# Kernel optimization log

Hardware: AMD Instinct MI355X
Metric: run time of the kernel (lower is better)

The kernel has to match this reference:

```python
import jax, jax.numpy as jnp
import numpy as np

MAX_INT = 1e4  # sentinel used by the original (transitions into START / out of STOP forbidden)
VOCAB, E, H, T, B, S = 50257, 512, 1024, 50, 8, 512  # T = tagset_size + 2


def _lstm_scan(x, h0, c0, Wih, Whh, b):
    # x: [time, batch, E] (time axis is the ORIGINAL batch dim, faithful to the
    # torch code which feeds [B,S,E] into a batch_first=False LSTM)
    def step(carry, xt):
        h, c = carry
        g = xt @ Wih.T + h @ Whh.T + b
        i, f, gg, o = jnp.split(g, 4, axis=-1)  # torch gate order i,f,g,o
        c = jax.nn.sigmoid(f) * c + jax.nn.sigmoid(i) * jnp.tanh(gg)
        h = jax.nn.sigmoid(o) * jnp.tanh(c)
        return (h, c), h
    _, hs = jax.lax.scan(step, (h0, c0), x)
    return hs


def setup_inputs() -> dict:
    key = jax.random.key(0)
    k = jax.random.split(key, 14)
    Hd = H // 2
    X = jax.random.randint(k[0], (B, S), 0, VOCAB)
    Y = jax.random.randint(k[1], (B, S), 0, T - 2)  # real tags only (no start/stop)
    h0 = jax.random.normal(k[2], (2, S, Hd), jnp.float32)
    c0 = jax.random.normal(k[3], (2, S, Hd), jnp.float32)
    emb_table = jax.random.normal(k[4], (VOCAB, E), jnp.float32) * 0.02
    Wih_f = jax.random.normal(k[5], (4 * Hd, E), jnp.float32) * 0.05
    Whh_f = jax.random.normal(k[6], (4 * Hd, Hd), jnp.float32) * 0.05
    b_f = jnp.zeros((4 * Hd,), jnp.float32)
    Wih_b = jax.random.normal(k[7], (4 * Hd, E), jnp.float32) * 0.05
    Whh_b = jax.random.normal(k[8], (4 * Hd, Hd), jnp.float32) * 0.05
    b_b = jnp.zeros((4 * Hd,), jnp.float32)
    fc_W = jax.random.normal(k[9], (T, H), jnp.float32) * 0.05
    fc_b = jnp.zeros((T,), jnp.float32)
    tr = jax.random.normal(k[10], (T, T), jnp.float32)
    transitions = tr.at[-2, :].set(-MAX_INT).at[:, -1].set(-MAX_INT)
    return {"X": X, "Y": Y, "h0": h0, "c0": c0, "emb_table": emb_table,
            "Wih_f": Wih_f, "Whh_f": Whh_f, "b_f": b_f,
            "Wih_b": Wih_b, "Whh_b": Whh_b, "b_b": b_b,
            "fc_W": fc_W, "fc_b": fc_b, "transitions": transitions}


def reference(X, Y, h0, c0, emb_table, Wih_f, Whh_f, b_f, Wih_b, Whh_b, b_b, fc_W, fc_b, transitions):
    emb = emb_table[X]                                   # [B,S,E]
    # BiLSTM: torch sees axis0 as time (faithful quirk), hidden batch == S
    hf = _lstm_scan(emb, h0[0], c0[0], Wih_f, Whh_f, b_f)
    hb = _lstm_scan(emb[::-1], h0[1], c0[1], Wih_b, Whh_b, b_b)[::-1]
    lstm_out = jnp.concatenate([hf, hb], axis=-1)        # [B,S,H]
    feats = lstm_out @ fc_W.T + fc_b                     # [B,S,T]
    nB, Tt = X.shape[0], transitions.shape[0]
    # CRF forward algorithm (log partition), vectorized over tags
    init = jnp.full((nB, Tt), -MAX_INT, feats.dtype).at[:, -2].set(0.0)
    def crf_step(fv, feat):                              # fv [B,T], feat [B,T]
        nv = fv[:, None, :] + transitions[None, :, :] + feat[:, :, None]  # [B,next,prev]
        return jax.nn.logsumexp(nv, axis=2), None
    fv, _ = jax.lax.scan(crf_step, init, jnp.swapaxes(feats, 0, 1))
    forward_score = jax.nn.logsumexp(fv + transitions[-1][None, :], axis=1).sum()
    # gold path score
    start = jnp.full((nB, 1), Tt - 2, dtype=Y.dtype)
    tags = jnp.concatenate([start, Y], axis=1)           # [B,S+1]
    trans_sc = transitions[tags[:, 1:], tags[:, :-1]].sum()
    emit_sc = jnp.take_along_axis(feats, tags[:, 1:, None], axis=2)[..., 0].sum()
    gold_score = trans_sc + emit_sc + transitions[-1, tags[:, -1]].sum()
    score = forward_score - gold_score
    return score, Y
```

## Files before the change

kernel.cpp:

```cpp
#include <hip/hip_runtime.h>
#include <hip/hip_bf16.h>

typedef __attribute__((ext_vector_type(4))) float f32x4;
typedef __attribute__((ext_vector_type(8))) short short8;

#define LN2F 0.69314718055994531f

__device__ __forceinline__ unsigned short f2b(float x){
  union{float f;unsigned u;}v; v.f=x;
  unsigned r = v.u + 0x7fffu + ((v.u>>16)&1u);
  return (unsigned short)(r>>16);
}
__device__ __forceinline__ float b2f(unsigned short h){
  union{unsigned u;float f;}v; v.u = ((unsigned)h)<<16; return v.f;
}
__device__ __forceinline__ float sigm(float x){ return 1.f/(1.f+__expf(-x)); }
__device__ __forceinline__ float tanh_(float x){ float t=__expf(2.f*x); return 1.f - 2.f/(t+1.f); }

__device__ __forceinline__ void gll16(const void* g, void* l){
  __builtin_amdgcn_global_load_lds((const __attribute__((address_space(1))) void*)g,
                                   (__attribute__((address_space(3))) void*)l, 16, 0, 0);
}

__global__ __launch_bounds__(256) void prep_kernel(
  const int* __restrict__ X, const int* __restrict__ Y,
  const float* __restrict__ h0, const float* __restrict__ c0,
  const float* __restrict__ emb,
  const float* __restrict__ WihF, const float* __restrict__ WihB,
  const float* __restrict__ WhhFf, const float* __restrict__ WhhBf,
  const float* __restrict__ fcWf, const float* __restrict__ trans,
  unsigned short* __restrict__ Abf, unsigned short* __restrict__ Wcat,
  unsigned short* __restrict__ WhhF, unsigned short* __restrict__ WhhB,
  unsigned short* __restrict__ hbufs, float* __restrict__ cbuf,
  unsigned short* __restrict__ fcW, unsigned short* __restrict__ Ebf,
  float* __restrict__ out)
{
  const int tid = blockIdx.x*256 + threadIdx.x;
  const int nth = gridDim.x*256;
  if(tid==0) out[0] = 0.f;
  for(int i=tid;i<524288;i+=nth){
    int r = i>>7, q = i&127;
    float4 v = ((const float4*)(emb + (size_t)X[r]*512))[q];
    ushort4 o; o.x=f2b(v.x); o.y=f2b(v.y); o.z=f2b(v.z); o.w=f2b(v.w);
    ((ushort4*)Abf)[i] = o;
  }
  for(int i=tid;i<524288;i+=nth){
    int r = i>>7, q = i&127;
    const float* src = (r<2048) ? (WihF + (size_t)r*512) : (WihB + (size_t)(r-2048)*512);
    float4 v = ((const float4*)src)[q];
    ushort4 o; o.x=f2b(v.x); o.y=f2b(v.y); o.z=f2b(v.z); o.w=f2b(v.w);
    ((ushort4*)Wcat)[i] = o;
  }
  for(int i=tid;i<262144;i+=nth){
    float4 v = ((const float4*)WhhFf)[i];
    ushort4 o; o.x=f2b(v.x); o.y=f2b(v.y); o.z=f2b(v.z); o.w=f2b(v.w);
    ((ushort4*)WhhF)[i] = o;
  }
  for(int i=tid;i<262144;i+=nth){
    float4 v = ((const float4*)WhhBf)[i];
    ushort4 o; o.x=f2b(v.x); o.y=f2b(v.y); o.z=f2b(v.z); o.w=f2b(v.w);
    ((ushort4*)WhhB)[i] = o;
  }
  for(int i=tid;i<131072;i+=nth){
    int d = i>>16, rest = i&65535;
    float4 v = ((const float4*)h0)[i];
    ushort4 o; o.x=f2b(v.x); o.y=f2b(v.y); o.z=f2b(v.z); o.w=f2b(v.w);
    ((ushort4*)hbufs)[(size_t)(d*2)*65536 + rest] = o;
  }
  for(int i=tid;i<131072;i+=nth) ((float4*)cbuf)[i] = ((const float4*)c0)[i];
  for(int i=tid;i<16384;i+=nth){
    int n = i>>8, q = i&255;
    float4 v;
    if (n<50) v = ((const float4*)(fcWf + (size_t)n*1024))[q];
    else { v.x=0.f; v.y=0.f; v.z=0.f; v.w=0.f; }
    ushort4 o; o.x=f2b(v.x); o.y=f2b(v.y); o.z=f2b(v.z); o.w=f2b(v.w);
    ((ushort4*)fcW)[i] = o;
  }
  for(int i=tid;i<4096;i+=nth){
    int n = i>>6, p = i&63;
    float v = (n<50 && p<50) ? __expf(trans[n*50+p]) : 0.f;
    Ebf[i] = f2b(v);
  }
  for(int i=tid;i<4096;i+=nth) out[1+i] = (float)Y[i];
}

__global__ __launch_bounds__(256) void gemm1_kernel(const unsigned short* __restrict__ A,
                                                    const unsigned short* __restrict__ B,
                                                    unsigned short* __restrict__ C){
  __shared__ __align__(16) unsigned short As[2][128*32];
  __shared__ __align__(16) unsigned short Bs[2][128*32];
  const int t = threadIdx.x, w = t>>6, l = t&63;
  const int m0 = blockIdx.x<<7, n0 = blockIdx.y<<7;
  const int wr = (w>>1)<<6, wc = (w&1)<<6;
  const int fr = l&15, fk = (l>>4)<<3;
  f32x4 acc[4][4];
  #pragma unroll
  for(int i=0;i<4;i++)
    #pragma unroll
    for(int j=0;j<4;j++) acc[i][j]=(f32x4)0.f;
  const unsigned short* Ab = A + (size_t)m0*512;
  const unsigned short* Bb = B + (size_t)n0*512;
  const int r0 = (w<<5) + (l>>2);
  const int c0 = (l&3)<<3;
  const int wo = (w<<5)*32;
  gll16(Ab + (size_t)r0*512 + c0,      As[0] + wo);
  gll16(Ab + (size_t)(r0+16)*512 + c0, As[0] + wo + 16*32);
  gll16(Bb + (size_t)r0*512 + c0,      Bs[0] + wo);
  gll16(Bb + (size_t)(r0+16)*512 + c0, Bs[0] + wo + 16*32);
  asm volatile("s_waitcnt vmcnt(0)" ::: "memory");
  __syncthreads();
  int cur = 0;
  for(int kt=0; kt<16; ++kt){
    if(kt<15){
      const int kc = ((kt+1)<<5) + c0;
      gll16(Ab + (size_t)r0*512 + kc,      As[cur^1] + wo);
      gll16(Ab + (size_t)(r0+16)*512 + kc, As[cur^1] + wo + 16*32);
      gll16(Bb + (size_t)r0*512 + kc,      Bs[cur^1] + wo);
      gll16(Bb + (size_t)(r0+16)*512 + kc, Bs[cur^1] + wo + 16*32);
    }
    short8 af[4], bf[4];
    #pragma unroll
    for(int mi=0;mi<4;mi++) af[mi] = *(const short8*)&As[cur][(wr+mi*16+fr)*32 + fk];
    #pragma unroll
    for(int ni=0;ni<4;ni++) bf[ni] = *(const short8*)&Bs[cur][(wc+ni*16+fr)*32 + fk];
    #pragma unroll
    for(int mi=0;mi<4;mi++)
      #pragma unroll
      for(int ni=0;ni<4;ni++)
        acc[mi][ni] = __builtin_amdgcn_mfma_f32_16x16x32_bf16(af[mi], bf[ni], acc[mi][ni], 0,0,0);
    asm volatile("s_waitcnt vmcnt(0)" ::: "memory");
    __syncthreads();
    cur ^= 1;
  }
  #pragma unroll
  for(int mi=0;mi<4;mi++)
    #pragma unroll
    for(int ni=0;ni<4;ni++)
      #pragma unroll
      for(int j=0;j<4;j++){
        int row = m0 + wr + mi*16 + ((l>>4)<<2) + j;
        int col = n0 + wc + ni*16 + fr;
        C[(size_t)row*4096 + col] = f2b(acc[mi][ni][j]);
      }
}

__global__ __launch_bounds__(256) void lstm_step_kernel(
  unsigned short* __restrict__ hbufs, float* __restrict__ cbuf,
  unsigned short* __restrict__ hall, const unsigned short* __restrict__ Gin,
  const unsigned short* __restrict__ WhhF_, const unsigned short* __restrict__ WhhB_,
  const float* __restrict__ bF, const float* __restrict__ bB, int t)
{
  __shared__ __align__(16) unsigned short WL[16*4*64*8];
  __shared__ __align__(16) unsigned short Ab4[4][128*32];
  const int d = blockIdx.z;
  const int m0 = blockIdx.x<<7;
  const int u0 = blockIdx.y<<4;
  const int tin = d ? (7-t) : t;
  const int par = t&1;
  const unsigned short* hprev = hbufs + (size_t)(d*2+par)*262144;
  unsigned short* hnext = hbufs + (size_t)(d*2+(par^1))*262144;
  const unsigned short* W = d ? WhhB_ : WhhF_;
  const float* bias = d ? bB : bF;
  const int tx = threadIdx.x, w = tx>>6, l = tx&63;
  const int fr = l&15, q = l>>4, fk = q<<3;
  {
    const int row = tx >> 2, qq = tx & 3;
    const int g = row >> 4, ul = row & 15;
    const int grow = (g<<9) + u0 + ul;
    #pragma unroll
    for(int kt=0;kt<16;kt++){
      uint4 v = *(const uint4*)(W + (size_t)grow*512 + kt*32 + qq*8);
      *(uint4*)(WL + ((kt*4+g)*64 + (qq*16+ul))*8) = v;
    }
  }
  __syncthreads();
  f32x4 acc[2][4];
  #pragma unroll
  for(int i=0;i<2;i++)
    #pragma unroll
    for(int j=0;j<4;j++) acc[i][j]=(f32x4)0.f;
  const int r0 = (w<<5) + (l>>2), c0 = (l&3)<<3;
  const unsigned short* hA0 = hprev + (size_t)(m0+r0)*512;
  const unsigned short* hA1 = hprev + (size_t)(m0+r0+16)*512;
#define ABUF(i) (Ab4[(i)] + ((w<<5)*32))
  gll16(hA0 + 0*32 + c0, ABUF(0)); gll16(hA1 + 0*32 + c0, ABUF(0)+16*32);
  gll16(hA0 + 1*32 + c0, ABUF(1)); gll16(hA1 + 1*32 + c0, ABUF(1)+16*32);
  gll16(hA0 + 2*32 + c0, ABUF(2)); gll16(hA1 + 2*32 + c0, ABUF(2)+16*32);
  gll16(hA0 + 3*32 + c0, ABUF(3)); gll16(hA1 + 3*32 + c0, ABUF(3)+16*32);
#define LSTEP(KT, VM) {                                                       \
    if((KT)+4 < 16){                                                          \
      const int kc_ = ((KT)+4)*32 + c0;                                       \
      gll16(hA0 + kc_, ABUF(((KT)+4)&3));                                     \
      gll16(hA1 + kc_, ABUF(((KT)+4)&3)+16*32);                               \
    }                                                                         \
    asm volatile("s_waitcnt vmcnt(" VM ")" ::: "memory");                     \
    const unsigned short* cur_ = ABUF((KT)&3);                                \
    short8 a0_ = *(const short8*)(cur_ + fr*32 + fk);                         \
    short8 a1_ = *(const short8*)(cur_ + (16+fr)*32 + fk);                    \
    short8 bv_[4];                                                            \
    _Pragma("unroll")                                                         \
    for(int g=0;g<4;g++) bv_[g] = *(const short8*)(WL + (((KT)*4+g)*64 + l)*8);\
    _Pragma("unroll")                                                         \
    for(int g=0;g<4;g++){                                                     \
      acc[0][g] = __builtin_amdgcn_mfma_f32_16x16x32_bf16(a0_, bv_[g], acc[0][g], 0,0,0); \
      acc[1][g] = __builtin_amdgcn_mfma_f32_16x16x32_bf16(a1_, bv_[g], acc[1][g], 0,0,0); \
    }                                                                         \
  }
  LSTEP(0,"8")  LSTEP(1,"8")  LSTEP(2,"8")  LSTEP(3,"8")
  LSTEP(4,"8")  LSTEP(5,"8")  LSTEP(6,"8")  LSTEP(7,"8")
  LSTEP(8,"8")  LSTEP(9,"8")  LSTEP(10,"8") LSTEP(11,"8")
  LSTEP(12,"6") LSTEP(13,"4") LSTEP(14,"2") LSTEP(15,"0")
#undef LSTEP
#undef ABUF
  #pragma unroll
  for(int mi=0;mi<2;mi++)
    #pragma unroll
    for(int j=0;j<4;j++){
      int rs = m0 + w*32 + mi*16 + (q<<2) + j;
      int u  = u0 + fr;
      size_t grow = (size_t)(tin*512 + rs)*4096 + (size_t)d*2048;
      float p0 = acc[mi][0][j] + b2f(Gin[grow +    0 + u]) + bias[   0+u];
      float p1 = acc[mi][1][j] + b2f(Gin[grow +  512 + u]) + bias[ 512+u];
      float p2 = acc[mi][2][j] + b2f(Gin[grow + 1024 + u]) + bias[1024+u];
      float p3 = acc[mi][3][j] + b2f(Gin[grow + 1536 + u]) + bias[1536+u];
      size_t ci = (size_t)d*262144 + (size_t)rs*512 + u;
      float c = sigm(p1)*cbuf[ci] + sigm(p0)*tanh_(p2);
      cbuf[ci] = c;
      float h = sigm(p3)*tanh_(c);
      hnext[(size_t)rs*512+u] = f2b(h);
      hall[(size_t)(tin*512+rs)*1024 + (size_t)d*512 + u] = f2b(h);
    }
}

__global__ __launch_bounds__(256) void fc_kernel(const unsigned short* __restrict__ hA,
    const unsigned short* __restrict__ Wf, const float* __restrict__ fcb,
    float* __restrict__ feats){
  __shared__ __align__(16) unsigned short As[128*40];
  __shared__ __align__(16) unsigned short Bs[64*40];
  const int tx = threadIdx.x, w = tx>>6, l = tx&63;
  const int m0 = blockIdx.x<<7;
  const int srow = tx>>2, scol = (tx&3)<<3;
  const int fr=l&15, fk=(l>>4)<<3;
  f32x4 acc[2][4];
  #pragma unroll
  for(int i=0;i<2;i++)
    #pragma unroll
    for(int j=0;j<4;j++) acc[i][j]=(f32x4)0.f;
  uint4 pa0 = *(const uint4*)(hA + (size_t)(m0+srow)*1024 + scol);
  uint4 pa1 = *(const uint4*)(hA + (size_t)(m0+64+srow)*1024 + scol);
  uint4 pb0 = *(const uint4*)(Wf + (size_t)srow*1024 + scol);
  for(int kt=0; kt<32; ++kt){
    __syncthreads();
    *(uint4*)&As[srow*40+scol] = pa0;
    *(uint4*)&As[(64+srow)*40+scol] = pa1;
    *(uint4*)&Bs[srow*40+scol] = pb0;
    __syncthreads();
    if(kt<31){
      int kc = (kt+1)*32 + scol;
      pa0 = *(const uint4*)(hA + (size_t)(m0+srow)*1024 + kc);
      pa1 = *(const uint4*)(hA + (size_t)(m0+64+srow)*1024 + kc);
      pb0 = *(const uint4*)(Wf + (size_t)srow*1024 + kc);
    }
    short8 af[2], bf[4];
    #pragma unroll
    for(int mi=0;mi<2;mi++) af[mi] = *(const short8*)&As[(w*32+mi*16+fr)*40 + fk];
    #pragma unroll
    for(int ni=0;ni<4;ni++) bf[ni] = *(const short8*)&Bs[(ni*16+fr)*40 + fk];
    #pragma unroll
    for(int mi=0;mi<2;mi++)
      #pragma unroll
      for(int ni=0;ni<4;ni++)
        acc[mi][ni] = __builtin_amdgcn_mfma_f32_16x16x32_bf16(af[mi], bf[ni], acc[mi][ni], 0,0,0);
  }
  #pragma unroll
  for(int mi=0;mi<2;mi++)
    #pragma unroll
    for(int ni=0;ni<4;ni++)
      #pragma unroll
      for(int j=0;j<4;j++){
        int rs = m0 + w*32 + mi*16 + ((l>>4)<<2) + j;
        int n  = ni*16 + fr;
        feats[(size_t)rs*64+n] = acc[mi][ni][j] + (n<50 ? fcb[n] : 0.f);
      }
}

__global__ __launch_bounds__(64) void crf_group_kernel(
    const float* __restrict__ feats, const unsigned short* __restrict__ Ebf,
    float* __restrict__ Wout, int* __restrict__ kexp)
{
  __shared__ __align__(16) unsigned short PT[64*72];
  __shared__ float fe[16*64];
  const int g = blockIdx.x, b = blockIdx.y;
  const int l = threadIdx.x;
  const int lj = l & 15, q = l >> 4;
  const float* fb = feats + (size_t)(b*512 + g*16)*64;
  #pragma unroll
  for(int j=0;j<16;j++) fe[j*64 + l] = fb[j*64 + l];
  short8 afE[4][2];
  #pragma unroll
  for(int i=0;i<4;i++)
    #pragma unroll
    for(int h=0;h<2;h++)
      afE[i][h] = *(const short8*)(Ebf + (i*16+lj)*64 + h*32 + q*8);
  {
    uint4 erow[8];
    #pragma unroll
    for(int i=0;i<8;i++) erow[i] = *(const uint4*)(Ebf + l*64 + i*8);
    float ef0 = __expf(fe[l]);
    const unsigned* e32 = (const unsigned*)erow;
    #pragma unroll
    for(int m=0;m<64;m++){
      unsigned short eb = (unsigned short)(e32[m>>1] >> ((m&1)*16));
      PT[m*72 + l] = f2b(b2f(eb) * ef0);
    }
  }
  float sc_lag = 1.f;
  int exprev = 0, kblk = 0;
  #pragma unroll
  for(int k=1;k<16;k++){
    kblk += exprev;
    float ev[4][4];
    #pragma unroll
    for(int i=0;i<4;i++)
      #pragma unroll
      for(int r=0;r<4;r++)
        ev[i][r] = __expf(fe[k*64 + i*16 + q*4 + r]) * sc_lag;
    short8 bfP[4][2];
    #pragma unroll
    for(int j=0;j<4;j++)
      #pragma unroll
      for(int h=0;h<2;h++)
        bfP[j][h] = *(const short8*)&PT[(j*16+lj)*72 + h*32 + q*8];
    f32x4 acc[4][4];
    #pragma unroll
    for(int i=0;i<4;i++)
      #pragma unroll
      for(int j=0;j<4;j++) acc[i][j] = (f32x4)0.f;
    #pragma unroll
    for(int h=0;h<2;h++)
      #pragma unroll
      for(int i=0;i<4;i++)
        #pragma unroll
        for(int j=0;j<4;j++)
          acc[i][j] = __builtin_amdgcn_mfma_f32_16x16x32_bf16(afE[i][h], bfP[j][h], acc[i][j], 0,0,0);
    float mx = 1e-30f;
    float* Wo = Wout + (size_t)(b*32 + g)*4096;
    #pragma unroll
    for(int i=0;i<4;i++)
      #pragma unroll
      for(int j=0;j<4;j++){
        float v0 = acc[i][j][0]*ev[i][0];
        float v1 = acc[i][j][1]*ev[i][1];
        float v2 = acc[i][j][2]*ev[i][2];
        float v3 = acc[i][j][3]*ev[i][3];
        mx = fmaxf(fmaxf(mx, fmaxf(v0,v1)), fmaxf(v2,v3));
        int base = (j*16+lj)*72 + i*16 + q*4;
        *(unsigned*)&PT[base]   = (unsigned)f2b(v0) | ((unsigned)f2b(v1)<<16);
        *(unsigned*)&PT[base+2] = (unsigned)f2b(v2) | ((unsigned)f2b(v3)<<16);
        if(k==15){
          int n = i*16 + q*4, m = j*16 + lj;
          Wo[(size_t)(n+0)*64 + m] = v0;
          Wo[(size_t)(n+1)*64 + m] = v1;
          Wo[(size_t)(n+2)*64 + m] = v2;
          Wo[(size_t)(n+3)*64 + m] = v3;
        }
      }
    #pragma unroll
    for(int off=1; off<64; off<<=1) mx = fmaxf(mx, __shfl_xor(mx, off));
    int ex = ((__builtin_bit_cast(int, mx) >> 23) & 0xff) - 127;
    ex = ex < -120 ? -120 : (ex > 120 ? 120 : ex);
    sc_lag = __builtin_bit_cast(float, (unsigned)((127-ex)<<23));
    exprev = ex;
  }
  if(l==0) kexp[b*32 + g] = kblk;
}

__global__ __launch_bounds__(256) void crf_seq_kernel(const float* __restrict__ W,
    const int* __restrict__ kexp, const float* __restrict__ trans,
    const float* __restrict__ feats, const int* __restrict__ Y,
    float* __restrict__ out){
  const int b = blockIdx.x;
  if(b < 8){
    if(threadIdx.x >= 64) return;
    __shared__ __align__(16) float sh[64];
    const int l = threadIdx.x;
    const float* Wb = W + (size_t)b*131072;
    float kl = (l<32) ? (float)kexp[b*32 + l] : 0.f;
    #pragma unroll
    for(int off=32;off;off>>=1) kl += __shfl_down(kl, off);
    float G = (l==48) ? 1.f : 0.f;
    float sc = 1.f, Mrun = 0.f;
    int exprev = 0;
    float4 curA[16], curB[16];
    #pragma unroll
    for(int i=0;i<16;i++) curA[i] = ((const float4*)(Wb + (size_t)l*64))[i];

#define SEQ_STEP(CUR, NXT, GI) {                                            \
    sh[l] = G;                                                              \
    const float* wn = Wb + (size_t)(((GI)+1)&31)*4096 + (size_t)l*64;       \
    _Pragma("unroll")                                                       \
    for(int i=0;i<16;i++) NXT[i] = ((const float4*)wn)[i];                  \
    float4 gq[16];                                                          \
    _Pragma("unroll")                                                       \
    for(int i=0;i<16;i++) gq[i] = ((const float4*)sh)[i];                   \
    float a0=0.f,a1=0.f,a2=0.f,a3=0.f;                                      \
    _Pragma("unroll")                                                       \
    for(int i=0;i<16;i++){                                                  \
      a0 = fmaf(CUR[i].x, gq[i].x, a0);                                     \
      a1 = fmaf(CUR[i].y, gq[i].y, a1);                                     \
      a2 = fmaf(CUR[i].z, gq[i].z, a2);                                     \
      a3 = fmaf(CUR[i].w, gq[i].w, a3);                                     \
    }                                                                       \
    float S = (a0+a1)+(a2+a3);                                              \
    Mrun += (float)exprev;                                                  \
    G = S * sc;                                                             \
    float Sp = __builtin_bit_cast(float, __builtin_amdgcn_readfirstlane(    \
                 __builtin_bit_cast(int, fmaxf(S, 1e-35f))));               \
    int ex = ((__builtin_bit_cast(int, Sp) >> 23) & 0xff) - 127;            \
    ex = ex < -120 ? -120 : (ex > 120 ? 120 : ex);                          \
    sc = __builtin_bit_cast(float, (unsigned)((127-ex)<<23));               \
    exprev = ex;                                                            \
  }

    for(int g=0; g<32; g+=2){
      SEQ_STEP(curA, curB, g)
      SEQ_STEP(curB, curA, g+1)
    }
#undef SEQ_STEP
    float u = (l<50) ? __expf(trans[49*50+l]) : 0.f;
    float val = G * u;
    #pragma unroll
    for(int off=32;off;off>>=1) val += __shfl_down(val, off);
    if(l==0) atomicAdd(out, logf(fmaxf(val,1e-35f)) + (Mrun + kl)*LN2F);
  } else {
    const int tx = threadIdx.x;
    float acc = 0.f;
    for(int i=tx; i<4096; i+=256){
      int s = i & 511;
      int y = Y[i];
      int prev = s ? Y[i-1] : 48;
      acc += trans[y*50+prev] + feats[(size_t)i*64+y];
      if (s==511) acc += trans[49*50+y];
    }
    #pragma unroll
    for(int off=32; off; off>>=1) acc += __shfl_down(acc, off);
    __shared__ float red[4];
    if((tx&63)==0) red[tx>>6] = acc;
    __syncthreads();
    if(tx==0) atomicAdd(out, -(red[0]+red[1]+red[2]+red[3]));
  }
}

extern "C" void kernel_launch(void* const* d_in, const int* in_sizes, int n_in,
                              void* d_out, int out_size, void* d_ws, size_t ws_size,
                              hipStream_t stream) {
  (void)in_sizes; (void)n_in; (void)out_size; (void)ws_size;
  const int*   X     = (const int*)d_in[0];
  const int*   Y     = (const int*)d_in[1];
  const float* h0    = (const float*)d_in[2];
  const float* c0    = (const float*)d_in[3];
  const float* emb   = (const float*)d_in[4];
  const float* WihF  = (const float*)d_in[5];
  const float* WhhFf = (const float*)d_in[6];
  const float* bF    = (const float*)d_in[7];
  const float* WihB  = (const float*)d_in[8];
  const float* WhhBf = (const float*)d_in[9];
  const float* bB    = (const float*)d_in[10];
  const float* fcWf  = (const float*)d_in[11];
  const float* fcb   = (const float*)d_in[12];
  const float* trans = (const float*)d_in[13];
  float* out = (float*)d_out;
  char* ws = (char*)d_ws;

  unsigned short* Abf   = (unsigned short*)(ws + 0);
  unsigned short* Wcat  = (unsigned short*)(ws + 4194304);
  unsigned short* WhhF  = (unsigned short*)(ws + 8388608);
  unsigned short* WhhB  = (unsigned short*)(ws + 10485760);
  unsigned short* Gin   = (unsigned short*)(ws + 12582912);
  float*          Wgrp  = (float*)(ws + 12582912);
  int*            kexp  = (int*)(ws + 20971520);
  unsigned short* hbufs = (unsigned short*)(ws + 46137344);
  float*          cbuf  = (float*)(ws + 48234496);
  unsigned short* hall  = (unsigned short*)(ws + 50331648);
  unsigned short* fcW   = (unsigned short*)(ws + 58720256);
  float*          feats = (float*)(ws + 58851328);
  unsigned short* Ebf   = (unsigned short*)(ws + 59900160);

  hipLaunchKernelGGL(prep_kernel, dim3(1024), dim3(256), 0, stream,
      X, Y, h0, c0, emb, WihF, WihB, WhhFf, WhhBf, fcWf, trans,
      Abf, Wcat, WhhF, WhhB, hbufs, cbuf, fcW, Ebf, out);
  hipLaunchKernelGGL(gemm1_kernel, dim3(32,32), dim3(256), 0, stream, Abf, Wcat, Gin);
  for(int t=0;t<8;t++)
    hipLaunchKernelGGL(lstm_step_kernel, dim3(4,32,2), dim3(256), 0, stream,
        hbufs, cbuf, hall, Gin, WhhF, WhhB, bF, bB, t);
  hipLaunchKernelGGL(fc_kernel, dim3(32), dim3(256), 0, stream, hall, fcW, fcb, feats);
  hipLaunchKernelGGL(crf_group_kernel, dim3(32,8), dim3(64), 0, stream, feats, Ebf, Wgrp, kexp);
  hipLaunchKernelGGL(crf_seq_kernel, dim3(9), dim3(256), 0, stream, Wgrp, kexp, trans, feats, Y, out);
}
```

Measured before the change: 189.4 us.

## Deepen gemm1 pipeline with per-wave buffers, adjust LSTM prefetch, regroup CRF chunks

The input-projection GEMM now gives each wave its own 4-deep LDS ring and issues loads three stages ahead. This removes the block-wide __syncthreads and keeps more loads in flight, at the cost of each wave loading its own 64-row A and B panels instead of sharing 128-row tiles. The LSTM step prefetch depth drops from 4 to 3 stages. The CRF group kernel now processes 32-step chunks in 16 groups rather than 16-step chunks in 32 groups, which halves the serial steps in the sequential combine kernel but lengthens each group's serial chain.

```diff
diff --git a/kernel.cpp b/kernel.cpp
--- a/kernel.cpp
+++ b/kernel.cpp
@@ -87,51 +87,55 @@
 __global__ __launch_bounds__(256) void gemm1_kernel(const unsigned short* __restrict__ A,
                                                     const unsigned short* __restrict__ B,
                                                     unsigned short* __restrict__ C){
-  __shared__ __align__(16) unsigned short As[2][128*32];
-  __shared__ __align__(16) unsigned short Bs[2][128*32];
+  __shared__ __align__(16) unsigned short SS[4][4][2][2048];
   const int t = threadIdx.x, w = t>>6, l = t&63;
   const int m0 = blockIdx.x<<7, n0 = blockIdx.y<<7;
   const int wr = (w>>1)<<6, wc = (w&1)<<6;
   const int fr = l&15, fk = (l>>4)<<3;
+  const int sr = l>>2, c0 = (l&3)<<3;
   f32x4 acc[4][4];
   #pragma unroll
   for(int i=0;i<4;i++)
     #pragma unroll
     for(int j=0;j<4;j++) acc[i][j]=(f32x4)0.f;
-  const unsigned short* Ab = A + (size_t)m0*512;
-  const unsigned short* Bb = B + (size_t)n0*512;
-  const int r0 = (w<<5) + (l>>2);
-  const int c0 = (l&3)<<3;
-  const int wo = (w<<5)*32;
-  gll16(Ab + (size_t)r0*512 + c0,      As[0] + wo);
-  gll16(Ab + (size_t)(r0+16)*512 + c0, As[0] + wo + 16*32);
-  gll16(Bb + (size_t)r0*512 + c0,      Bs[0] + wo);
-  gll16(Bb + (size_t)(r0+16)*512 + c0, Bs[0] + wo + 16*32);
-  asm volatile("s_waitcnt vmcnt(0)" ::: "memory");
-  __syncthreads();
-  int cur = 0;
-  for(int kt=0; kt<16; ++kt){
-    if(kt<15){
-      const int kc = ((kt+1)<<5) + c0;
-      gll16(Ab + (size_t)r0*512 + kc,      As[cur^1] + wo);
-      gll16(Ab + (size_t)(r0+16)*512 + kc, As[cur^1] + wo + 16*32);
-      gll16(Bb + (size_t)r0*512 + kc,      Bs[cur^1] + wo);
-      gll16(Bb + (size_t)(r0+16)*512 + kc, Bs[cur^1] + wo + 16*32);
-    }
-    short8 af[4], bf[4];
-    #pragma unroll
-    for(int mi=0;mi<4;mi++) af[mi] = *(const short8*)&As[cur][(wr+mi*16+fr)*32 + fk];
-    #pragma unroll
-    for(int ni=0;ni<4;ni++) bf[ni] = *(const short8*)&Bs[cur][(wc+ni*16+fr)*32 + fk];
-    #pragma unroll
-    for(int mi=0;mi<4;mi++)
-      #pragma unroll
-      for(int ni=0;ni<4;ni++)
-        acc[mi][ni] = __builtin_amdgcn_mfma_f32_16x16x32_bf16(af[mi], bf[ni], acc[mi][ni], 0,0,0);
-    asm volatile("s_waitcnt vmcnt(0)" ::: "memory");
-    __syncthreads();
-    cur ^= 1;
-  }
+  const unsigned short* Aw = A + (size_t)(m0+wr)*512;
+  const unsigned short* Bw = B + (size_t)(n0+wc)*512;
+#define G1STAGE(KT) { \
+    unsigned short* pa_ = &SS[w][(KT)&3][0][0]; \
+    unsigned short* pb_ = &SS[w][(KT)&3][1][0]; \
+    const int kc_ = ((KT)<<5) + c0; \
+    gll16(Aw + (size_t)(    sr)*512 + kc_, pa_); \
+    gll16(Aw + (size_t)(16+sr)*512 + kc_, pa_+512); \
+    gll16(Aw + (size_t)(32+sr)*512 + kc_, pa_+1024); \
+    gll16(Aw + (size_t)(48+sr)*512 + kc_, pa_+1536); \
+    gll16(Bw + (size_t)(    sr)*512 + kc_, pb_); \
+    gll16(Bw + (size_t)(16+sr)*512 + kc_, pb_+512); \
+    gll16(Bw + (size_t)(32+sr)*512 + kc_, pb_+1024); \
+    gll16(Bw + (size_t)(48+sr)*512 + kc_, pb_+1536); \
+  }
+  G1STAGE(0) G1STAGE(1) G1STAGE(2)
+#define G1STEP(KT, VM) { \
+    if((KT)+3 < 16) G1STAGE((KT)+3) \
+    asm volatile("s_waitcnt vmcnt(" VM ")" ::: "memory"); \
+    const unsigned short* pa_ = &SS[w][(KT)&3][0][0]; \
+    const unsigned short* pb_ = &SS[w][(KT)&3][1][0]; \
+    short8 af_[4], bf_[4]; \
+    _Pragma("unroll") \
+    for(int mi=0;mi<4;mi++) af_[mi] = *(const short8*)(pa_ + mi*512 + fr*32 + fk); \
+    _Pragma("unroll") \
+    for(int ni=0;ni<4;ni++) bf_[ni] = *(const short8*)(pb_ + ni*512 + fr*32 + fk); \
+    _Pragma("unroll") \
+    for(int mi=0;mi<4;mi++) \
+      _Pragma("unroll") \
+      for(int ni=0;ni<4;ni++) \
+        acc[mi][ni] = __builtin_amdgcn_mfma_f32_16x16x32_bf16(af_[mi], bf_[ni], acc[mi][ni], 0,0,0); \
+  }
+  G1STEP(0,"24")  G1STEP(1,"24")  G1STEP(2,"24")  G1STEP(3,"24")
+  G1STEP(4,"24")  G1STEP(5,"24")  G1STEP(6,"24")  G1STEP(7,"24")
+  G1STEP(8,"24")  G1STEP(9,"24")  G1STEP(10,"24") G1STEP(11,"24")
+  G1STEP(12,"24") G1STEP(13,"16") G1STEP(14,"8")  G1STEP(15,"0")
+#undef G1STEP
+#undef G1STAGE
   #pragma unroll
   for(int mi=0;mi<4;mi++)
     #pragma unroll
@@ -186,12 +190,11 @@
   gll16(hA0 + 0*32 + c0, ABUF(0)); gll16(hA1 + 0*32 + c0, ABUF(0)+16*32);
   gll16(hA0 + 1*32 + c0, ABUF(1)); gll16(hA1 + 1*32 + c0, ABUF(1)+16*32);
   gll16(hA0 + 2*32 + c0, ABUF(2)); gll16(hA1 + 2*32 + c0, ABUF(2)+16*32);
-  gll16(hA0 + 3*32 + c0, ABUF(3)); gll16(hA1 + 3*32 + c0, ABUF(3)+16*32);
 #define LSTEP(KT, VM) {                                                       \
-    if((KT)+4 < 16){                                                          \
-      const int kc_ = ((KT)+4)*32 + c0;                                       \
-      gll16(hA0 + kc_, ABUF(((KT)+4)&3));                                     \
-      gll16(hA1 + kc_, ABUF(((KT)+4)&3)+16*32);                               \
+    if((KT)+3 < 16){                                                          \
+      const int kc_ = ((KT)+3)*32 + c0;                                       \
+      gll16(hA0 + kc_, ABUF(((KT)+3)&3));                                     \
+      gll16(hA1 + kc_, ABUF(((KT)+3)&3)+16*32);                               \
     }                                                                         \
     asm volatile("s_waitcnt vmcnt(" VM ")" ::: "memory");                     \
     const unsigned short* cur_ = ABUF((KT)&3);                                \
@@ -206,9 +209,9 @@
       acc[1][g] = __builtin_amdgcn_mfma_f32_16x16x32_bf16(a1_, bv_[g], acc[1][g], 0,0,0); \
     }                                                                         \
   }
-  LSTEP(0,"8")  LSTEP(1,"8")  LSTEP(2,"8")  LSTEP(3,"8")
-  LSTEP(4,"8")  LSTEP(5,"8")  LSTEP(6,"8")  LSTEP(7,"8")
-  LSTEP(8,"8")  LSTEP(9,"8")  LSTEP(10,"8") LSTEP(11,"8")
+  LSTEP(0,"6")  LSTEP(1,"6")  LSTEP(2,"6")  LSTEP(3,"6")
+  LSTEP(4,"6")  LSTEP(5,"6")  LSTEP(6,"6")  LSTEP(7,"6")
+  LSTEP(8,"6")  LSTEP(9,"6")  LSTEP(10,"6") LSTEP(11,"6")
   LSTEP(12,"6") LSTEP(13,"4") LSTEP(14,"2") LSTEP(15,"0")
 #undef LSTEP
 #undef ABUF
@@ -289,13 +292,13 @@
     float* __restrict__ Wout, int* __restrict__ kexp)
 {
   __shared__ __align__(16) unsigned short PT[64*72];
-  __shared__ float fe[16*64];
+  __shared__ float fe[32*64];
   const int g = blockIdx.x, b = blockIdx.y;
   const int l = threadIdx.x;
   const int lj = l & 15, q = l >> 4;
-  const float* fb = feats + (size_t)(b*512 + g*16)*64;
-  #pragma unroll
-  for(int j=0;j<16;j++) fe[j*64 + l] = fb[j*64 + l];
+  const float* fb = feats + (size_t)(b*512 + g*32)*64;
+  #pragma unroll
+  for(int j=0;j<32;j++) fe[j*64 + l] = fb[j*64 + l];
   short8 afE[4][2];
   #pragma unroll
   for(int i=0;i<4;i++)
@@ -316,8 +319,7 @@
   }
   float sc_lag = 1.f;
   int exprev = 0, kblk = 0;
-  #pragma unroll
-  for(int k=1;k<16;k++){
+  for(int k=1;k<32;k++){
     kblk += exprev;
     float ev[4][4];
     #pragma unroll
@@ -344,7 +346,7 @@
         for(int j=0;j<4;j++)
           acc[i][j] = __builtin_amdgcn_mfma_f32_16x16x32_bf16(afE[i][h], bfP[j][h], acc[i][j], 0,0,0);
     float mx = 1e-30f;
-    float* Wo = Wout + (size_t)(b*32 + g)*4096;
+    float* Wo = Wout + (size_t)(b*16 + g)*4096;
     #pragma unroll
     for(int i=0;i<4;i++)
       #pragma unroll
@@ -357,7 +359,7 @@
         int base = (j*16+lj)*72 + i*16 + q*4;
         *(unsigned*)&PT[base]   = (unsigned)f2b(v0) | ((unsigned)f2b(v1)<<16);
         *(unsigned*)&PT[base+2] = (unsigned)f2b(v2) | ((unsigned)f2b(v3)<<16);
-        if(k==15){
+        if(k==31){
           int n = i*16 + q*4, m = j*16 + lj;
           Wo[(size_t)(n+0)*64 + m] = v0;
           Wo[(size_t)(n+1)*64 + m] = v1;
@@ -372,7 +374,7 @@
     sc_lag = __builtin_bit_cast(float, (unsigned)((127-ex)<<23));
     exprev = ex;
   }
-  if(l==0) kexp[b*32 + g] = kblk;
+  if(l==0) kexp[b*16 + g] = kblk;
 }
 
 __global__ __launch_bounds__(256) void crf_seq_kernel(const float* __restrict__ W,
@@ -384,8 +386,8 @@
     if(threadIdx.x >= 64) return;
     __shared__ __align__(16) float sh[64];
     const int l = threadIdx.x;
-    const float* Wb = W + (size_t)b*131072;
-    float kl = (l<32) ? (float)kexp[b*32 + l] : 0.f;
+    const float* Wb = W + (size_t)b*65536;
+    float kl = (l<16) ? (float)kexp[b*16 + l] : 0.f;
     #pragma unroll
     for(int off=32;off;off>>=1) kl += __shfl_down(kl, off);
     float G = (l==48) ? 1.f : 0.f;
@@ -397,7 +399,7 @@
 
 #define SEQ_STEP(CUR, NXT, GI) {                                            \
     sh[l] = G;                                                              \
-    const float* wn = Wb + (size_t)(((GI)+1)&31)*4096 + (size_t)l*64;       \
+    const float* wn = Wb + (size_t)(((GI)+1)&15)*4096 + (size_t)l*64;       \
     _Pragma("unroll")                                                       \
     for(int i=0;i<16;i++) NXT[i] = ((const float4*)wn)[i];                  \
     float4 gq[16];                                                          \
@@ -422,7 +424,7 @@
     exprev = ex;                                                            \
   }
 
-    for(int g=0; g<32; g+=2){
+    for(int g=0; g<16; g+=2){
       SEQ_STEP(curA, curB, g)
       SEQ_STEP(curB, curA, g+1)
     }
@@ -494,6 +496,6 @@
     hipLaunchKernelGGL(lstm_step_kernel, dim3(4,32,2), dim3(256), 0, stream,
         hbufs, cbuf, hall, Gin, WhhF, WhhB, bF, bB, t);
   hipLaunchKernelGGL(fc_kernel, dim3(32), dim3(256), 0, stream, hall, fcW, fcb, feats);
-  hipLaunchKernelGGL(crf_group_kernel, dim3(32,8), dim3(64), 0, stream, feats, Ebf, Wgrp, kexp);
+  hipLaunchKernelGGL(crf_group_kernel, dim3(16,8), dim3(64), 0, stream, feats, Ebf, Wgrp, kexp);
   hipLaunchKernelGGL(crf_seq_kernel, dim3(9), dim3(256), 0, stream, Wgrp, kexp, trans, feats, Y, out);
 }
```

New measurement: 192.5 us. About the same (+1.6%).
